# Kernel tuning notes

Hardware: AMD Instinct MI355X
Metric: run time of the kernel (lower is better)

Reference implementation:

```python
import jax, jax.numpy as jnp
import numpy as np

B, N, T, D, DG, DS, NC = 16, 64, 256, 64, 64, 9, 2

def _pe(times, d, max_len):
    # PositionalEncodingTF: timescales = max_len ** linspace(0,1,d//2)
    ts = jnp.asarray(max_len ** np.linspace(0.0, 1.0, d // 2), jnp.float32)
    st = times[..., None] / ts
    return jnp.concatenate([jnp.sin(st), jnp.cos(st)], -1)

def _ln(h, g, b):
    m = h.mean(-1, keepdims=True)
    v = ((h - m) ** 2).mean(-1, keepdims=True)
    return (h - m) * jax.lax.rsqrt(v + 1e-5) * g + b

def setup_inputs():
    key = jax.random.key(0)
    ks = jax.random.split(key, 40)
    s = 0.02
    value = jax.random.normal(ks[0], (B, T, N))
    obs = (jax.random.uniform(ks[1], (B, T, N)) < 0.5).astype(jnp.float32)
    times = jnp.sort(jax.random.uniform(ks[2], (B, T)) * T, axis=1)
    F = D + 2 * DG  # per-node GRU input feature size [x_t, h, time_enc]
    return dict(
        x=jnp.concatenate([value, obs, times[..., None]], -1),
        nufft=jax.random.normal(ks[3], (B, 2, T, N)),
        delta_t=jax.random.uniform(ks[4], (B, T)) * 0.1,
        static=jax.random.normal(ks[5], (B, DS)),
        lengths=jax.random.randint(ks[6], (B,), 1, T + 1),
        proj_w=jax.random.normal(ks[7], (2, D)) * s, proj_b=jnp.zeros(D),
        Wqkv=jax.random.normal(ks[8], (D, 3 * D)) * s, bqkv=jnp.zeros(3 * D),
        Wo=jax.random.normal(ks[9], (D, D)) * s, bo=jnp.zeros(D),
        ln1_g=jnp.ones(D), ln1_b=jnp.zeros(D),
        W1=jax.random.normal(ks[10], (D, D)) * s, b1=jnp.zeros(D),
        W2=jax.random.normal(ks[11], (D, D)) * s, b2=jnp.zeros(D),
        ln2_g=jnp.ones(D), ln2_b=jnp.zeros(D),
        WQ_f=jax.random.normal(ks[12], (T, T)) * 0.05,
        WK_f=jax.random.normal(ks[13], (T, T)) * 0.05,
        Wz=jax.random.normal(ks[14], (2 * F, DG)) * s, bz=jnp.zeros(DG),
        Wr=jax.random.normal(ks[15], (2 * F, DG)) * s, br=jnp.zeros(DG),
        Wc=jax.random.normal(ks[16], (2 * F, DG)) * s, bc=jnp.zeros(DG),
        Wfin=jax.random.normal(ks[17], (DG,)) * s, bfin=jnp.zeros(()),
        We=jax.random.normal(ks[18], (DS, N)) * s, be=jnp.zeros(N),
        Wc1=jax.random.normal(ks[19], (2 * N, 200)) * s, bc1=jnp.zeros(200),
        Wc2=jax.random.normal(ks[20], (200, NC)) * s, bc2=jnp.zeros(NC),
    )

def _forward(x, nufft, delta_t, static, lengths, proj_w, proj_b, Wqkv, bqkv, Wo, bo,
             ln1_g, ln1_b, W1, b1, W2, b2, ln2_g, ln2_b, WQ_f, WK_f,
             Wz, bz, Wr, br, Wc, bc, Wfin, bfin, We, be, Wc1, bc1, Wc2, bc2):
    lengths = jnp.maximum(lengths, 1)
    value = x[:, :, :N].transpose(0, 2, 1)          # (B,N,T)
    obs = x[:, :, N:2 * N].transpose(0, 2, 1)       # (B,N,T) observation mask
    times = x[:, :, -1]                              # (B,T)
    # Conv2d(2->D, 1x1) input projection == per-element linear over [value, mask]
    feat = jnp.stack([value, obs], -1) @ proj_w + proj_b   # (B,N,T,D)
    pe1 = _pe(times, D, T)                           # (B,T,D)
    tin = feat + pe1[:, None]                        # (B,N,T,D)
    # single-head transformer encoder layer (post-norm, relu FFN, eval: no dropout)
    qkv = tin @ Wqkv + bqkv
    q, k, v = jnp.split(qkv, 3, -1)
    scores = jnp.einsum('bnqd,bnkd->bnqk', q, k) / jnp.sqrt(jnp.float32(D))
    kpad = jnp.arange(T)[None, :] >= lengths[:, None]      # (B,T) key padding
    scores = jnp.where(kpad[:, None, None, :], -1e9, scores)
    attn = jax.nn.softmax(scores, -1)
    ao = jnp.einsum('bnqk,bnkd->bnqd', attn, v) @ Wo + bo
    h1 = _ln(tin + ao, ln1_g, ln1_b)
    ff = jax.nn.relu(h1 @ W1 + b1) @ W2 + b2
    tout = _ln(h1 + ff, ln2_g, ln2_b)
    m = obs[..., None]
    x_tat = m * tin + (1.0 - m) * tout               # masked blend (B,N,T,D)
    # Variable_Attention_layer on nufft channel 1: relu-score softmax attention
    xf = nufft[:, 1].transpose(0, 2, 1)              # (B,N,T)
    S = jax.nn.relu(jnp.einsum('bnt,bmt->bnm', xf @ WQ_f, xf @ WK_f)) / jnp.sqrt(jnp.float32(T))
    A = jax.nn.softmax(S, -1).mean(0)                # (N,N)
    A = 0.5 * (A + A.T)
    sm = jax.nn.softmax(A, -1)
    A = 0.5 * (sm + sm.T)
    pe2 = _pe(times, DG, T)                          # (B,T,DG)
    # graph-conv GRU over time (CGRNN) with delta_t decay + length masking
    def stepf(h, inputs):
        xt, tet, dtt, t = inputs                     # (B,N,D),(B,DG),(B,),()
        h = h * jnp.exp(-jax.nn.relu(dtt))[:, None, None]
        te = jnp.broadcast_to(tet[:, None, :], (h.shape[0], N, DG))
        inp = jnp.concatenate([xt, h, te], -1)
        gin = jnp.concatenate([inp, jnp.einsum('nm,bmf->bnf', A, inp)], -1)
        z = jax.nn.sigmoid(gin @ Wz + bz)
        r = jax.nn.sigmoid(gin @ Wr + br)
        inc = jnp.concatenate([xt, r * h, te], -1)
        cin = jnp.concatenate([inc, jnp.einsum('nm,bmf->bnf', A, inc)], -1)
        c = jnp.tanh(cin @ Wc + bc)
        hn = z * h + (1.0 - z) * c
        h = jnp.where((t < lengths)[:, None, None], hn, h)
        return h, None
    h0 = jnp.zeros((x.shape[0], N, DG), x.dtype)
    xs = (x_tat.transpose(2, 0, 1, 3), pe2.transpose(1, 0, 2), delta_t.T, jnp.arange(T))
    hT, _ = jax.lax.scan(stepf, h0, xs)
    out = hT @ Wfin + bfin                           # final 1x1 conv -> (B,N)
    emb = static @ We + be                           # (B,N)
    hcl = jax.nn.relu(jnp.concatenate([out, emb], -1) @ Wc1 + bc1)
    return hcl @ Wc2 + bc2                           # (B,NC)

def reference(x, nufft, delta_t, static, lengths, proj_w, proj_b, Wqkv, bqkv, Wo, bo,
              ln1_g, ln1_b, W1, b1, W2, b2, ln2_g, ln2_b, WQ_f, WK_f,
              Wz, bz, Wr, br, Wc, bc, Wfin, bfin, We, be, Wc1, bc1, Wc2, bc2):
    return _forward(x, nufft, delta_t, static, lengths, proj_w, proj_b, Wqkv, bqkv, Wo, bo,
                    ln1_g, ln1_b, W1, b1, W2, b2, ln2_g, ln2_b, WQ_f, WK_f,
                    Wz, bz, Wr, br, Wc, bc, Wfin, bfin, We, be, Wc1, bc1, Wc2, bc2)
```

## Files before the change

kernel.cpp:

```cpp
#include <hip/hip_runtime.h>
#include <hip/hip_bf16.h>
#include <cmath>

#define DEV __device__ __forceinline__

typedef short s16x8 __attribute__((ext_vector_type(8)));
typedef float f32x4 __attribute__((ext_vector_type(4)));

DEV unsigned short f2bu(float x){
  __hip_bfloat16 h = __float2bfloat16(x);
  return *reinterpret_cast<unsigned short*>(&h);
}
DEV float bs2f(unsigned short v){ return __uint_as_float(((unsigned)v)<<16); }
DEV float bs2f(short v){ return bs2f((unsigned short)v); }

DEV int swzo(int row, int col){
  return (row*128 + ((col*2) ^ ((row&7)<<4))) >> 1;
}
DEV s16x8 ldfrag(const short* tile, int t16, int lane, int kk){
  int row = t16 + (lane & 15);
  int c0  = (kk<<5) + ((lane>>4)<<3);
  int off = (row*128 + ((c0<<1) ^ ((row&7)<<4))) >> 1;
  return *(const s16x8*)(tile + off);
}
DEV int swzv(int d, int t){
  return (d*512 + ((t*2) ^ ((d&7)<<4))) >> 1;
}

__global__ void k0_prep(const float* __restrict__ Wqkv, const float* __restrict__ Wo,
                        const float* __restrict__ W1, const float* __restrict__ W2,
                        short* __restrict__ Wqkv_t, short* __restrict__ Wo_t,
                        short* __restrict__ W1_t, short* __restrict__ W2_t)
{
  int t = blockIdx.x*256 + threadIdx.x;
  if (t < 12288){ int nn=t>>6, k=t&63; Wqkv_t[t]=(short)f2bu(Wqkv[k*192+nn]); }
  else if (t < 16384){ int e=t-12288; int nn=e>>6,k=e&63; Wo_t[e]=(short)f2bu(Wo[k*64+nn]); }
  else if (t < 20480){ int e=t-16384; int nn=e>>6,k=e&63; W1_t[e]=(short)f2bu(W1[k*64+nn]); }
  else if (t < 24576){ int e=t-20480; int nn=e>>6,k=e&63; W2_t[e]=(short)f2bu(W2[k*64+nn]); }
}

__global__ void k1_pe_u(const float* __restrict__ x, const float* __restrict__ delta_t,
                        const float* __restrict__ Wz, const float* __restrict__ bz,
                        const float* __restrict__ Wr, const float* __restrict__ br,
                        const float* __restrict__ Wc, const float* __restrict__ bc,
                        float* __restrict__ pe, float* __restrict__ U, float* __restrict__ decay)
{
  const int bt = blockIdx.x;
  const int d  = threadIdx.x;
  __shared__ float pes[64];
  float tmv = x[(size_t)bt*129 + 128];
  int j = d & 31;
  float ts = (float)pow(256.0, (double)j * (1.0/31.0));
  float st = tmv / ts;
  float v = (d < 32) ? sinf(st) : cosf(st);
  pes[d] = v;
  pe[(size_t)bt*64 + d] = v;
  __syncthreads();
  float a0=bz[d], a1=0.f, a2=br[d], a3=0.f, a4=bc[d], a5=0.f;
  for (int k=0;k<64;k++){
    float p = pes[k];
    a0 = fmaf(p, Wz[(128+k)*64+d], a0);
    a1 = fmaf(p, Wz[(320+k)*64+d], a1);
    a2 = fmaf(p, Wr[(128+k)*64+d], a2);
    a3 = fmaf(p, Wr[(320+k)*64+d], a3);
    a4 = fmaf(p, Wc[(128+k)*64+d], a4);
    a5 = fmaf(p, Wc[(320+k)*64+d], a5);
  }
  float* u = U + (size_t)bt*384;
  u[d]=a0; u[64+d]=a1; u[128+d]=a2; u[192+d]=a3; u[256+d]=a4; u[320+d]=a5;
  if (d==0) decay[bt] = expf(-fmaxf(delta_t[bt], 0.f));
}

__global__ void k2a_qfkf(const float* __restrict__ nufft, const float* __restrict__ WQf,
                         const float* __restrict__ WKf, float* __restrict__ qf, float* __restrict__ kf)
{
  const int bn = blockIdx.x, b = bn>>6, n = bn&63;
  const int u = threadIdx.x;
  __shared__ float xs[256];
  xs[u] = nufft[ ((((size_t)b*2)+1)*256 + u)*64 + n ];
  __syncthreads();
  float aq=0.f, ak=0.f;
  for (int t=0;t<256;t++){
    float xv = xs[t];
    aq = fmaf(xv, WQf[t*256+u], aq);
    ak = fmaf(xv, WKf[t*256+u], ak);
  }
  qf[(size_t)bn*256+u]=aq;
  kf[(size_t)bn*256+u]=ak;
}

__launch_bounds__(256, 1)
__global__ void k2b_soft(const float* __restrict__ qf, const float* __restrict__ kf,
                         float* __restrict__ soft)
{
  const int b = blockIdx.x, tid = threadIdx.x;
  __shared__ float qs[64*257];
  __shared__ float ksh[64*257];
  __shared__ float Ss[64*65];
  const float* qb = qf + ((size_t)b<<14);
  const float* kb = kf + ((size_t)b<<14);
  for (int e=tid; e<16384; e+=256){
    int r=e>>8, c=e&255;
    qs[r*257+c]=qb[e];
    ksh[r*257+c]=kb[e];
  }
  __syncthreads();
  const int n = tid>>2, m0 = (tid&3)<<4;
  float acc[16];
  #pragma unroll
  for (int i=0;i<16;i++) acc[i]=0.f;
  for (int t=0;t<256;t++){
    float qv = qs[n*257+t];
    #pragma unroll
    for (int i=0;i<16;i++) acc[i] = fmaf(qv, ksh[(m0+i)*257+t], acc[i]);
  }
  #pragma unroll
  for (int i=0;i<16;i++) Ss[n*65+m0+i] = fmaxf(acc[i],0.f)*(1.f/16.f);
  __syncthreads();
  if (tid < 64){
    float mx=-1e30f;
    for (int m=0;m<64;m++) mx=fmaxf(mx, Ss[tid*65+m]);
    float s=0.f;
    for (int m=0;m<64;m++) s += expf(Ss[tid*65+m]-mx);
    float inv=1.f/s;
    for (int m=0;m<64;m++) soft[((size_t)b<<12)+(tid<<6)+m] = expf(Ss[tid*65+m]-mx)*inv;
  }
}

__global__ void k2c_A(const float* __restrict__ soft, short* __restrict__ Abf,
                      float* __restrict__ rs_out)
{
  const int tid = threadIdx.x;
  __shared__ float A0[64*65];
  __shared__ float A1[64*65];
  for (int e=tid; e<4096; e+=256){
    int nn=e>>6, mm=e&63;
    float s=0.f;
    #pragma unroll
    for (int b=0;b<16;b++) s += soft[((size_t)b<<12)+e];
    A0[nn*65+mm] = s*(1.f/16.f);
  }
  __syncthreads();
  for (int e=tid; e<4096; e+=256){
    int nn=e>>6, mm=e&63;
    A1[nn*65+mm] = 0.5f*(A0[nn*65+mm]+A0[mm*65+nn]);
  }
  __syncthreads();
  if (tid < 64){
    float mx=-1e30f;
    for (int m=0;m<64;m++) mx=fmaxf(mx, A1[tid*65+m]);
    float s=0.f;
    for (int m=0;m<64;m++) s += expf(A1[tid*65+m]-mx);
    float inv=1.f/s;
    for (int m=0;m<64;m++) A0[tid*65+m] = expf(A1[tid*65+m]-mx)*inv;
  }
  __syncthreads();
  for (int e=tid; e<4096; e+=256){
    int nn=e>>6, mm=e&63;
    float a = 0.5f*(A0[nn*65+mm]+A0[mm*65+nn]);
    A1[nn*65+mm] = a;
    Abf[e] = (short)f2bu(a);
  }
  __syncthreads();
  if (tid < 64){
    float s=0.f;
    for (int m=0;m<64;m++) s += A1[tid*65+m];
    rs_out[tid]=s;
  }
}

__launch_bounds__(512, 1)
__global__ void k3_former(const float* __restrict__ x, const float* __restrict__ pe_g,
    const float* __restrict__ proj_w, const float* __restrict__ proj_b,
    const short* __restrict__ Wqkv_t, const float* __restrict__ bqkv,
    const short* __restrict__ Wo_t, const float* __restrict__ bo,
    const float* __restrict__ ln1g, const float* __restrict__ ln1b,
    const short* __restrict__ W1_t, const float* __restrict__ b1,
    const short* __restrict__ W2_t, const float* __restrict__ b2,
    const float* __restrict__ ln2g, const float* __restrict__ ln2b,
    const int* __restrict__ lengths, unsigned short* __restrict__ xtat)
{
  const int bn = blockIdx.x, b = bn>>6, n = bn&63;
  const int tid = threadIdx.x, w = tid>>6, lane = tid&63;
  const int l15 = lane&15, lhi = lane>>4;
  __shared__ short tp_s[16384];
  __shared__ short q_s[16384];
  __shared__ short k_s[16384];
  __shared__ short v_t[16384];
  __shared__ float valr[256], obsr[256];

  int len = lengths[b]; if (len<1) len=1;
  const int LT = (len+15)>>4;
  const int KB = (len+63)>>6;

  if (tid < 256){
    const float* xr = x + ((size_t)b*256+tid)*129;
    valr[tid]=xr[n]; obsr[tid]=xr[64+n];
  }
  for (int e=tid; e<16384; e+=512) v_t[e]=0;
  __syncthreads();

  const int nrows = LT<<4;
  for (int e=tid; e<(nrows<<6); e+=512){
    int t=e>>6, d=e&63;
    float ti = fmaf(valr[t],proj_w[d], fmaf(obsr[t],proj_w[64+d], proj_b[d]))
             + pe_g[(((size_t)b<<8)+t)*64+d];
    tp_s[swzo(t,d)] = (short)f2bu(ti);
  }
  __syncthreads();

  #pragma unroll
  for (int j=0;j<2;j++){
    const int rt = w + (j<<3);
    if (rt < LT){
      s16x8 a0 = ldfrag(tp_s, rt<<4, lane, 0);
      s16x8 a1 = ldfrag(tp_s, rt<<4, lane, 1);
      const int rb = (rt<<4) + (lhi<<2);
      #pragma unroll
      for (int nt=0; nt<12; nt++){
        const short* wb = Wqkv_t + (((nt<<4)+l15)<<6) + (lhi<<3);
        s16x8 b0 = *(const s16x8*)wb;
        s16x8 b1v = *(const s16x8*)(wb+32);
        float bias = bqkv[(nt<<4)+l15];
        f32x4 acc = {bias,bias,bias,bias};
        acc = __builtin_amdgcn_mfma_f32_16x16x32_bf16(a0,b0,acc,0,0,0);
        acc = __builtin_amdgcn_mfma_f32_16x16x32_bf16(a1,b1v,acc,0,0,0);
        const int col = ((nt&3)<<4) + l15;
        if (nt<4){
          #pragma unroll
          for(int i=0;i<4;i++) q_s[swzo(rb+i,col)] = (short)f2bu(acc[i]*0.125f);
        } else if (nt<8){
          #pragma unroll
          for(int i=0;i<4;i++) k_s[swzo(rb+i,col)] = (short)f2bu(acc[i]);
        } else {
          #pragma unroll
          for(int i=0;i<4;i++) v_t[swzv(col, rb+i)] = (short)f2bu(acc[i]);
        }
      }
    }
  }
  __syncthreads();

  f32x4 Oac[2][4];
  float rsum[2][4];
  #pragma unroll
  for(int j=0;j<2;j++)
    #pragma unroll
    for(int dt=0;dt<4;dt++) Oac[j][dt]=(f32x4){0.f,0.f,0.f,0.f};
  #pragma unroll
  for(int j=0;j<2;j++)
    #pragma unroll
    for(int i=0;i<4;i++) rsum[j][i]=0.f;

  for (int kb=0; kb<KB; kb++){
    s16x8 kf[4][2];
    #pragma unroll
    for (int ct=0;ct<4;ct++){
      kf[ct][0]=ldfrag(k_s, (((kb<<2)+ct)<<4), lane, 0);
      kf[ct][1]=ldfrag(k_s, (((kb<<2)+ct)<<4), lane, 1);
    }
    #pragma unroll
    for (int j=0;j<2;j++){
      const int rt=w+(j<<3);
      if (rt < LT){
        s16x8 q0=ldfrag(q_s, rt<<4, lane, 0);
        s16x8 q1=ldfrag(q_s, rt<<4, lane, 1);
        const int rb=(rt<<4)+(lhi<<2);
        #pragma unroll
        for (int ct=0;ct<4;ct++){
          f32x4 s={0.f,0.f,0.f,0.f};
          s=__builtin_amdgcn_mfma_f32_16x16x32_bf16(q0,kf[ct][0],s,0,0,0);
          s=__builtin_amdgcn_mfma_f32_16x16x32_bf16(q1,kf[ct][1],s,0,0,0);
          const int key=(kb<<6)+(ct<<4)+l15;
          #pragma unroll
          for(int i=0;i<4;i++){
            float p = (key<len) ? __expf(s[i]) : 0.f;
            rsum[j][i]+=p;
            tp_s[swzo(rb+i,(ct<<4)+l15)] = (short)f2bu(p);
          }
        }
      }
    }
    __syncthreads();
    s16x8 vf[4][2];
    #pragma unroll
    for (int dt=0;dt<4;dt++){
      const int d=(dt<<4)+l15;
      #pragma unroll
      for (int kk=0;kk<2;kk++){
        const int k0=(kk<<5)+(lhi<<3);
        vf[dt][kk] = *(const s16x8*)(v_t + swzv(d, (kb<<6)+k0));
      }
    }
    #pragma unroll
    for (int j=0;j<2;j++){
      const int rt=w+(j<<3);
      if (rt < LT){
        s16x8 p0=ldfrag(tp_s, rt<<4, lane, 0);
        s16x8 p1=ldfrag(tp_s, rt<<4, lane, 1);
        #pragma unroll
        for (int dt=0;dt<4;dt++){
          Oac[j][dt]=__builtin_amdgcn_mfma_f32_16x16x32_bf16(p0,vf[dt][0],Oac[j][dt],0,0,0);
          Oac[j][dt]=__builtin_amdgcn_mfma_f32_16x16x32_bf16(p1,vf[dt][1],Oac[j][dt],0,0,0);
        }
      }
    }
    __syncthreads();
  }

  float inv[2][4];
  #pragma unroll
  for(int j=0;j<2;j++)
    #pragma unroll
    for(int i=0;i<4;i++){
      float v=rsum[j][i];
      v += __shfl_xor(v,1); v += __shfl_xor(v,2); v += __shfl_xor(v,4); v += __shfl_xor(v,8);
      inv[j][i]=1.f/v;
    }

  #pragma unroll
  for (int j=0;j<2;j++){
    const int rt=w+(j<<3);
    if (rt < LT){
      const int rb=(rt<<4)+(lhi<<2);
      #pragma unroll
      for (int dt=0;dt<4;dt++)
        #pragma unroll
        for (int i=0;i<4;i++)
          q_s[swzo(rb+i,(dt<<4)+l15)] = (short)f2bu(Oac[j][dt][i]*inv[j][i]);
    }
  }
  __syncthreads();

  f32x4 h1[2][4];
  #pragma unroll
  for (int j=0;j<2;j++){
    const int rt=w+(j<<3);
    if (rt < LT){
      s16x8 a0=ldfrag(q_s, rt<<4, lane, 0);
      s16x8 a1=ldfrag(q_s, rt<<4, lane, 1);
      const int rb=(rt<<4)+(lhi<<2);
      #pragma unroll
      for (int dt=0;dt<4;dt++){
        const int col=(dt<<4)+l15;
        const short* wb = Wo_t + (col<<6) + (lhi<<3);
        s16x8 b0=*(const s16x8*)wb, b1v=*(const s16x8*)(wb+32);
        float bias=bo[col];
        f32x4 acc={bias,bias,bias,bias};
        acc=__builtin_amdgcn_mfma_f32_16x16x32_bf16(a0,b0,acc,0,0,0);
        acc=__builtin_amdgcn_mfma_f32_16x16x32_bf16(a1,b1v,acc,0,0,0);
        #pragma unroll
        for(int i=0;i<4;i++){
          const int row=rb+i;
          acc[i]+= fmaf(valr[row],proj_w[col], fmaf(obsr[row],proj_w[64+col], proj_b[col]))
                 + pe_g[(((size_t)b<<8)+row)*64+col];
        }
        h1[j][dt]=acc;
      }
      f32x4 mu, rsq;
      #pragma unroll
      for(int i=0;i<4;i++){
        float sv = h1[j][0][i]+h1[j][1][i]+h1[j][2][i]+h1[j][3][i];
        sv += __shfl_xor(sv,1); sv+=__shfl_xor(sv,2); sv+=__shfl_xor(sv,4); sv+=__shfl_xor(sv,8);
        mu[i]=sv*(1.f/64.f);
      }
      #pragma unroll
      for(int i=0;i<4;i++){
        float sv=0.f;
        #pragma unroll
        for(int dt=0;dt<4;dt++){ float c=h1[j][dt][i]-mu[i]; sv=fmaf(c,c,sv); }
        sv += __shfl_xor(sv,1); sv+=__shfl_xor(sv,2); sv+=__shfl_xor(sv,4); sv+=__shfl_xor(sv,8);
        rsq[i]=1.f/sqrtf(sv*(1.f/64.f)+1e-5f);
      }
      #pragma unroll
      for(int dt=0;dt<4;dt++){
        const int col=(dt<<4)+l15;
        float g=ln1g[col], bb=ln1b[col];
        #pragma unroll
        for(int i=0;i<4;i++){
          float hv=(h1[j][dt][i]-mu[i])*rsq[i]*g+bb;
          h1[j][dt][i]=hv;
          k_s[swzo(rb+i,col)] = (short)f2bu(hv);
        }
      }
    }
  }
  __syncthreads();

  #pragma unroll
  for (int j=0;j<2;j++){
    const int rt=w+(j<<3);
    if (rt < LT){
      s16x8 a0=ldfrag(k_s, rt<<4, lane, 0);
      s16x8 a1=ldfrag(k_s, rt<<4, lane, 1);
      const int rb=(rt<<4)+(lhi<<2);
      #pragma unroll
      for (int dt=0;dt<4;dt++){
        const int col=(dt<<4)+l15;
        const short* wb = W1_t + (col<<6)+(lhi<<3);
        s16x8 b0=*(const s16x8*)wb, b1v=*(const s16x8*)(wb+32);
        float bias=b1[col];
        f32x4 acc={bias,bias,bias,bias};
        acc=__builtin_amdgcn_mfma_f32_16x16x32_bf16(a0,b0,acc,0,0,0);
        acc=__builtin_amdgcn_mfma_f32_16x16x32_bf16(a1,b1v,acc,0,0,0);
        #pragma unroll
        for(int i=0;i<4;i++) tp_s[swzo(rb+i,col)]=(short)f2bu(fmaxf(acc[i],0.f));
      }
    }
  }
  __syncthreads();

  #pragma unroll
  for (int j=0;j<2;j++){
    const int rt=w+(j<<3);
    if (rt < LT){
      s16x8 a0=ldfrag(tp_s, rt<<4, lane, 0);
      s16x8 a1=ldfrag(tp_s, rt<<4, lane, 1);
      const int rb=(rt<<4)+(lhi<<2);
      f32x4 to[4];
      #pragma unroll
      for (int dt=0;dt<4;dt++){
        const int col=(dt<<4)+l15;
        const short* wb = W2_t + (col<<6)+(lhi<<3);
        s16x8 b0=*(const s16x8*)wb, b1v=*(const s16x8*)(wb+32);
        float bias=b2[col];
        f32x4 acc={bias,bias,bias,bias};
        acc=__builtin_amdgcn_mfma_f32_16x16x32_bf16(a0,b0,acc,0,0,0);
        acc=__builtin_amdgcn_mfma_f32_16x16x32_bf16(a1,b1v,acc,0,0,0);
        acc += h1[j][dt];
        to[dt]=acc;
      }
      f32x4 mu, rsq;
      #pragma unroll
      for(int i=0;i<4;i++){
        float sv = to[0][i]+to[1][i]+to[2][i]+to[3][i];
        sv += __shfl_xor(sv,1); sv+=__shfl_xor(sv,2); sv+=__shfl_xor(sv,4); sv+=__shfl_xor(sv,8);
        mu[i]=sv*(1.f/64.f);
      }
      #pragma unroll
      for(int i=0;i<4;i++){
        float sv=0.f;
        #pragma unroll
        for(int dt=0;dt<4;dt++){ float c=to[dt][i]-mu[i]; sv=fmaf(c,c,sv); }
        sv += __shfl_xor(sv,1); sv+=__shfl_xor(sv,2); sv+=__shfl_xor(sv,4); sv+=__shfl_xor(sv,8);
        rsq[i]=1.f/sqrtf(sv*(1.f/64.f)+1e-5f);
      }
      #pragma unroll
      for(int dt=0;dt<4;dt++){
        const int col=(dt<<4)+l15;
        float g=ln2g[col], bb=ln2b[col];
        #pragma unroll
        for(int i=0;i<4;i++){
          const int row=rb+i;
          if (row < len){
            float tv=(to[dt][i]-mu[i])*rsq[i]*g+bb;
            float tin = fmaf(valr[row],proj_w[col], fmaf(obsr[row],proj_w[64+col], proj_b[col]))
                      + pe_g[(((size_t)b<<8)+row)*64+col];
            float ob = obsr[row];
            xtat[((size_t)bn<<14)+(row<<6)+col] = f2bu(ob*tin + (1.f-ob)*tv);
          }
        }
      }
    }
  }
}

__launch_bounds__(512, 1)
__global__ void k4_scan(const unsigned short* __restrict__ xtat, const float* __restrict__ U,
                        const float* __restrict__ decay, const short* __restrict__ Abf,
                        const float* __restrict__ rs_g,
                        const float* __restrict__ Wz, const float* __restrict__ Wr,
                        const float* __restrict__ Wc,
                        const int* __restrict__ lengths, float* __restrict__ hT)
{
  const int b = blockIdx.x;
  const int tid = threadIdx.x;
  const int w = tid >> 6, lane = tid & 63;
  const int tn = w & 3, tm0 = (w >> 2) << 1;
  const int colg = (tn<<4) + (lane & 15);
  const int rsub = (lane >> 4) << 2;

  __shared__ short h_rm[4096], h_tp[4096], xt_rm[4096], xt_tp[4096];
  __shared__ short rh_rm[4096], rh_tp[4096], axt_s[4096], ah_s[4096], arh_s[4096];
  __shared__ float dec_s[256];
  __shared__ float rs_s[64];

  int len = lengths[b]; if (len < 1) len = 1;
  for (int e=tid; e<256; e+=512) dec_s[e] = decay[b*256+e];
  if (tid < 64) rs_s[tid] = rs_g[tid];

  s16x8 aA[2][2];
  #pragma unroll
  for (int ti=0;ti<2;ti++)
    #pragma unroll
    for (int kk=0;kk<2;kk++)
      aA[ti][kk] = *(const s16x8*)(Abf + (((tm0+ti)<<4) + (lane&15))*64 + (kk<<5) + ((lane>>4)<<3));

  s16x8 wf[12][2];
  {
    const float* Wg[3] = {Wz, Wr, Wc};
    const int offs[4] = {0, 64, 192, 256};
    #pragma unroll
    for (int g3=0; g3<3; g3++)
      #pragma unroll
      for (int s4=0; s4<4; s4++)
        #pragma unroll
        for (int kk=0; kk<2; kk++){
          s16x8 tf;
          int kb = (kk<<5) + ((lane>>4)<<3);
          #pragma unroll
          for (int j=0;j<8;j++)
            tf[j] = (short)f2bu(Wg[g3][(offs[s4]+kb+j)*64 + colg]);
          wf[g3*4+s4][kk] = tf;
        }
  }

  f32x4 hreg[2] = {{0.f,0.f,0.f,0.f},{0.f,0.f,0.f,0.f}};
  const int xn  = tid >> 3;
  const int xd0 = (tid & 7) << 3;
  __syncthreads();

  for (int t=0; t<256; t++){
    float dc = dec_s[t];
    #pragma unroll
    for (int ti=0;ti<2;ti++)
      #pragma unroll
      for (int i=0;i<4;i++) hreg[ti][i] *= dc;

    if (t < len){
      #pragma unroll
      for (int ti=0;ti<2;ti++){
        int rb = ((tm0+ti)<<4) + rsub;
        #pragma unroll
        for (int i=0;i<4;i++){
          short hv = (short)f2bu(hreg[ti][i]);
          h_rm[swzo(rb+i, colg)] = hv;
          h_tp[swzo(colg, rb+i)] = hv;
        }
      }
      {
        const s16x8 vv = *(const s16x8*)((const short*)xtat + (((size_t)(b*64+xn))*256 + t)*64 + xd0);
        *(s16x8*)(xt_rm + swzo(xn, xd0)) = vv;
        #pragma unroll
        for (int j=0;j<8;j++) xt_tp[swzo(xd0+j, xn)] = vv[j];
      }
      __syncthreads();

      {
        f32x4 ax[2] = {{0,0,0,0},{0,0,0,0}}, ahh[2] = {{0,0,0,0},{0,0,0,0}};
        #pragma unroll
        for (int kk=0;kk<2;kk++){
          s16x8 bx = ldfrag(xt_tp, tn<<4, lane, kk);
          s16x8 bh = ldfrag(h_tp,  tn<<4, lane, kk);
          #pragma unroll
          for (int ti=0;ti<2;ti++){
            ax[ti]  = __builtin_amdgcn_mfma_f32_16x16x32_bf16(aA[ti][kk], bx, ax[ti], 0,0,0);
            ahh[ti] = __builtin_amdgcn_mfma_f32_16x16x32_bf16(aA[ti][kk], bh, ahh[ti], 0,0,0);
          }
        }
        #pragma unroll
        for (int ti=0;ti<2;ti++){
          int rb = ((tm0+ti)<<4) + rsub;
          #pragma unroll
          for (int i=0;i<4;i++){
            axt_s[swzo(rb+i, colg)] = (short)f2bu(ax[ti][i]);
            ah_s [swzo(rb+i, colg)] = (short)f2bu(ahh[ti][i]);
          }
        }
      }
      __syncthreads();

      const float* ub = U + ((size_t)(b*256+t))*384;
      float u1z=ub[colg], u2z=ub[64+colg], u1r=ub[128+colg], u2r=ub[192+colg];
      float u1c=ub[256+colg], u2c=ub[320+colg];

      f32x4 gz[2] = {{0,0,0,0},{0,0,0,0}}, gr[2] = {{0,0,0,0},{0,0,0,0}};
      #pragma unroll
      for (int ti=0;ti<2;ti++){
        int rt = (tm0+ti)<<4;
        #pragma unroll
        for (int kk=0;kk<2;kk++){
          s16x8 fxt = ldfrag(xt_rm, rt, lane, kk);
          s16x8 fh  = ldfrag(h_rm,  rt, lane, kk);
          s16x8 fax = ldfrag(axt_s, rt, lane, kk);
          s16x8 fah = ldfrag(ah_s,  rt, lane, kk);
          gz[ti] = __builtin_amdgcn_mfma_f32_16x16x32_bf16(fxt, wf[0][kk], gz[ti], 0,0,0);
          gz[ti] = __builtin_amdgcn_mfma_f32_16x16x32_bf16(fh,  wf[1][kk], gz[ti], 0,0,0);
          gz[ti] = __builtin_amdgcn_mfma_f32_16x16x32_bf16(fax, wf[2][kk], gz[ti], 0,0,0);
          gz[ti] = __builtin_amdgcn_mfma_f32_16x16x32_bf16(fah, wf[3][kk], gz[ti], 0,0,0);
          gr[ti] = __builtin_amdgcn_mfma_f32_16x16x32_bf16(fxt, wf[4][kk], gr[ti], 0,0,0);
          gr[ti] = __builtin_amdgcn_mfma_f32_16x16x32_bf16(fh,  wf[5][kk], gr[ti], 0,0,0);
          gr[ti] = __builtin_amdgcn_mfma_f32_16x16x32_bf16(fax, wf[6][kk], gr[ti], 0,0,0);
          gr[ti] = __builtin_amdgcn_mfma_f32_16x16x32_bf16(fah, wf[7][kk], gr[ti], 0,0,0);
        }
      }
      f32x4 zz[2];
      #pragma unroll
      for (int ti=0;ti<2;ti++){
        int rb = ((tm0+ti)<<4) + rsub;
        #pragma unroll
        for (int i=0;i<4;i++){
          float rsv = rs_s[rb+i];
          float gzv = gz[ti][i] + u1z + rsv*u2z;
          float grv = gr[ti][i] + u1r + rsv*u2r;
          float zv = 1.f/(1.f+__expf(-gzv));
          float rv = 1.f/(1.f+__expf(-grv));
          zz[ti][i] = zv;
          short rhv = (short)f2bu(rv * hreg[ti][i]);
          rh_rm[swzo(rb+i, colg)] = rhv;
          rh_tp[swzo(colg, rb+i)] = rhv;
        }
      }
      __syncthreads();

      {
        f32x4 ar[2] = {{0,0,0,0},{0,0,0,0}};
        #pragma unroll
        for (int kk=0;kk<2;kk++){
          s16x8 brh = ldfrag(rh_tp, tn<<4, lane, kk);
          #pragma unroll
          for (int ti=0;ti<2;ti++)
            ar[ti] = __builtin_amdgcn_mfma_f32_16x16x32_bf16(aA[ti][kk], brh, ar[ti], 0,0,0);
        }
        #pragma unroll
        for (int ti=0;ti<2;ti++){
          int rb = ((tm0+ti)<<4) + rsub;
          #pragma unroll
          for (int i=0;i<4;i++)
            arh_s[swzo(rb+i, colg)] = (short)f2bu(ar[ti][i]);
        }
      }
      __syncthreads();

      {
        f32x4 gc[2] = {{0,0,0,0},{0,0,0,0}};
        #pragma unroll
        for (int ti=0;ti<2;ti++){
          int rt = (tm0+ti)<<4;
          #pragma unroll
          for (int kk=0;kk<2;kk++){
            s16x8 fxt = ldfrag(xt_rm, rt, lane, kk);
            s16x8 frh = ldfrag(rh_rm, rt, lane, kk);
            s16x8 fax = ldfrag(axt_s, rt, lane, kk);
            s16x8 far = ldfrag(arh_s, rt, lane, kk);
            gc[ti] = __builtin_amdgcn_mfma_f32_16x16x32_bf16(fxt, wf[8][kk],  gc[ti], 0,0,0);
            gc[ti] = __builtin_amdgcn_mfma_f32_16x16x32_bf16(frh, wf[9][kk],  gc[ti], 0,0,0);
            gc[ti] = __builtin_amdgcn_mfma_f32_16x16x32_bf16(fax, wf[10][kk], gc[ti], 0,0,0);
            gc[ti] = __builtin_amdgcn_mfma_f32_16x16x32_bf16(far, wf[11][kk], gc[ti], 0,0,0);
          }
        }
        #pragma unroll
        for (int ti=0;ti<2;ti++){
          int rb = ((tm0+ti)<<4) + rsub;
          #pragma unroll
          for (int i=0;i<4;i++){
            float rsv = rs_s[rb+i];
            float gcv = gc[ti][i] + u1c + rsv*u2c;
            float cv = 1.f - 2.f/(__expf(2.f*gcv)+1.f);
            float zv = zz[ti][i];
            hreg[ti][i] = zv*hreg[ti][i] + (1.f-zv)*cv;
          }
        }
      }
      __syncthreads();
    }
  }

  #pragma unroll
  for (int ti=0;ti<2;ti++){
    int rb = ((tm0+ti)<<4) + rsub;
    #pragma unroll
    for (int i=0;i<4;i++)
      hT[(((size_t)b<<6) + rb + i)*64 + colg] = hreg[ti][i];
  }
}

__global__ void k5_head(const float* __restrict__ hT, const float* __restrict__ Wfin,
                        const float* __restrict__ bfin,
                        const float* __restrict__ stat, const float* __restrict__ We,
                        const float* __restrict__ be,
                        const float* __restrict__ Wc1, const float* __restrict__ bc1,
                        const float* __restrict__ Wc2, const float* __restrict__ bc2,
                        float* __restrict__ out)
{
  const int b = blockIdx.x, tid = threadIdx.x;
  __shared__ float cat[128];
  __shared__ float hcl[200];
  if (tid < 64){
    const float* hr = hT + (((size_t)b<<6)+tid)*64;
    float a = bfin[0];
    #pragma unroll
    for (int d=0;d<64;d++) a = fmaf(hr[d], Wfin[d], a);
    cat[tid]=a;
  } else if (tid < 128){
    int nn = tid-64;
    float a = be[nn];
    #pragma unroll
    for (int k=0;k<9;k++) a = fmaf(stat[b*9+k], We[k*64+nn], a);
    cat[tid]=a;
  }
  __syncthreads();
  if (tid < 200){
    float a = bc1[tid];
    for (int k=0;k<128;k++) a = fmaf(cat[k], Wc1[k*200+tid], a);
    hcl[tid] = fmaxf(a, 0.f);
  }
  __syncthreads();
  if (tid < 2){
    float a = bc2[tid];
    for (int k=0;k<200;k++) a = fmaf(hcl[k], Wc2[k*2+tid], a);
    out[b*2+tid] = a;
  }
}

extern "C" void kernel_launch(void* const* d_in, const int* in_sizes, int n_in,
                              void* d_out, int out_size, void* d_ws, size_t ws_size,
                              hipStream_t stream)
{
  const float* x       = (const float*)d_in[0];
  const float* nufft   = (const float*)d_in[1];
  const float* delta_t = (const float*)d_in[2];
  const float* stat    = (const float*)d_in[3];
  const int*   lengths = (const int*)  d_in[4];
  const float* proj_w  = (const float*)d_in[5];
  const float* proj_b  = (const float*)d_in[6];
  const float* Wqkv    = (const float*)d_in[7];
  const float* bqkv    = (const float*)d_in[8];
  const float* Wo      = (const float*)d_in[9];
  const float* bo      = (const float*)d_in[10];
  const float* ln1g    = (const float*)d_in[11];
  const float* ln1b    = (const float*)d_in[12];
  const float* W1      = (const float*)d_in[13];
  const float* b1      = (const float*)d_in[14];
  const float* W2      = (const float*)d_in[15];
  const float* b2      = (const float*)d_in[16];
  const float* ln2g    = (const float*)d_in[17];
  const float* ln2b    = (const float*)d_in[18];
  const float* WQf     = (const float*)d_in[19];
  const float* WKf     = (const float*)d_in[20];
  const float* Wz      = (const float*)d_in[21];
  const float* bz      = (const float*)d_in[22];
  const float* Wr      = (const float*)d_in[23];
  const float* br      = (const float*)d_in[24];
  const float* Wc      = (const float*)d_in[25];
  const float* bc      = (const float*)d_in[26];
  const float* Wfin    = (const float*)d_in[27];
  const float* bfin    = (const float*)d_in[28];
  const float* We      = (const float*)d_in[29];
  const float* be      = (const float*)d_in[30];
  const float* Wc1     = (const float*)d_in[31];
  const float* bc1     = (const float*)d_in[32];
  const float* Wc2     = (const float*)d_in[33];
  const float* bc2     = (const float*)d_in[34];
  float* out = (float*)d_out;

  char* ws = (char*)d_ws;
  size_t o = 0;
  float* pe    = (float*)(ws+o); o += (size_t)4096*64*4;
  float* U     = (float*)(ws+o); o += (size_t)4096*384*4;
  float* decay = (float*)(ws+o); o += (size_t)4096*4;
  unsigned short* xtat = (unsigned short*)(ws+o); o += (size_t)1024*256*64*2;
  float* qf    = (float*)(ws+o); o += (size_t)1024*256*4;
  float* kf    = (float*)(ws+o); o += (size_t)1024*256*4;
  float* soft  = (float*)(ws+o); o += (size_t)16*4096*4;
  short* Abf   = (short*)(ws+o); o += (size_t)4096*2;
  float* rs    = (float*)(ws+o); o += (size_t)64*4;
  float* hT    = (float*)(ws+o); o += (size_t)16*64*64*4;
  short* Wqkv_t= (short*)(ws+o); o += (size_t)12288*2;
  short* Wo_t  = (short*)(ws+o); o += (size_t)4096*2;
  short* W1_t  = (short*)(ws+o); o += (size_t)4096*2;
  short* W2_t  = (short*)(ws+o); o += (size_t)4096*2;
  (void)ws_size; (void)in_sizes; (void)n_in; (void)out_size;

  hipLaunchKernelGGL(k0_prep,   dim3(96),   dim3(256), 0, stream,
                     Wqkv, Wo, W1, W2, Wqkv_t, Wo_t, W1_t, W2_t);
  hipLaunchKernelGGL(k1_pe_u,   dim3(4096), dim3(64),  0, stream,
                     x, delta_t, Wz, bz, Wr, br, Wc, bc, pe, U, decay);
  hipLaunchKernelGGL(k2a_qfkf,  dim3(1024), dim3(256), 0, stream,
                     nufft, WQf, WKf, qf, kf);
  hipLaunchKernelGGL(k2b_soft,  dim3(16),   dim3(256), 0, stream, qf, kf, soft);
  hipLaunchKernelGGL(k2c_A,     dim3(1),    dim3(256), 0, stream, soft, Abf, rs);
  hipLaunchKernelGGL(k3_former, dim3(1024), dim3(512), 0, stream,
                     x, pe, proj_w, proj_b, Wqkv_t, bqkv, Wo_t, bo, ln1g, ln1b,
                     W1_t, b1, W2_t, b2, ln2g, ln2b, lengths, xtat);
  hipLaunchKernelGGL(k4_scan,   dim3(16),   dim3(512), 0, stream,
                     xtat, U, decay, Abf, rs, Wz, Wr, Wc, lengths, hT);
  hipLaunchKernelGGL(k5_head,   dim3(16),   dim3(256), 0, stream,
                     hT, Wfin, bfin, stat, We, be, Wc1, bc1, Wc2, bc2, out);
}
```

Before: 1.069 ms.

## Hoist x-dependent GRU gate projections out of the sequential scan into a parallel kernel

A new kernel, k35_xg, computes the input-side gate contributions (x_t and A·x_t times the z, r and c weights) for all timesteps in parallel across 4096 blocks and writes them to a bf16 buffer. The sequential scan now only does the hidden-state MFMAs and prefetches the next step's precomputed gates and U terms into registers. It loops only to len and applies the remaining decay product at the end. It also drops one LDS round trip and uses vector stores for the transposes. This shortens the serial critical path of a kernel that runs only 16 blocks, at the cost of an extra ~100MB workspace buffer, a launch, and extra bf16 rounding of the precomputed gates.

```diff
diff --git a/kernel.cpp b/kernel.cpp
--- a/kernel.cpp
+++ b/kernel.cpp
@@ -5,6 +5,7 @@
 #define DEV __device__ __forceinline__
 
 typedef short s16x8 __attribute__((ext_vector_type(8)));
+typedef short s16x4 __attribute__((ext_vector_type(4)));
 typedef float f32x4 __attribute__((ext_vector_type(4)));
 
 DEV unsigned short f2bu(float x){
@@ -29,14 +30,23 @@
 
 __global__ void k0_prep(const float* __restrict__ Wqkv, const float* __restrict__ Wo,
                         const float* __restrict__ W1, const float* __restrict__ W2,
+                        const float* __restrict__ Wz, const float* __restrict__ Wr,
+                        const float* __restrict__ Wc,
                         short* __restrict__ Wqkv_t, short* __restrict__ Wo_t,
-                        short* __restrict__ W1_t, short* __restrict__ W2_t)
+                        short* __restrict__ W1_t, short* __restrict__ W2_t,
+                        short* __restrict__ Wg_t)
 {
   int t = blockIdx.x*256 + threadIdx.x;
   if (t < 12288){ int nn=t>>6, k=t&63; Wqkv_t[t]=(short)f2bu(Wqkv[k*192+nn]); }
   else if (t < 16384){ int e=t-12288; int nn=e>>6,k=e&63; Wo_t[e]=(short)f2bu(Wo[k*64+nn]); }
   else if (t < 20480){ int e=t-16384; int nn=e>>6,k=e&63; W1_t[e]=(short)f2bu(W1[k*64+nn]); }
   else if (t < 24576){ int e=t-20480; int nn=e>>6,k=e&63; W2_t[e]=(short)f2bu(W2[k*64+nn]); }
+  else if (t < 49152){
+    int e=t-24576;
+    int g=e>>13, rem=e&8191, s=rem>>12, rem2=rem&4095, c=rem2>>6, k=rem2&63;
+    const float* Wg = (g==0)?Wz:((g==1)?Wr:Wc);
+    Wg_t[e] = (short)f2bu(Wg[((s?192:0)+k)*64 + c]);
+  }
 }
 
 __global__ void k1_pe_u(const float* __restrict__ x, const float* __restrict__ delta_t,
@@ -50,7 +60,7 @@
   __shared__ float pes[64];
   float tmv = x[(size_t)bt*129 + 128];
   int j = d & 31;
-  float ts = (float)pow(256.0, (double)j * (1.0/31.0));
+  float ts = exp2f((float)j * (8.0f/31.0f));
   float st = tmv / ts;
   float v = (d < 32) ? sinf(st) : cosf(st);
   pes[d] = v;
@@ -465,8 +475,82 @@
   }
 }
 
+__global__ void k35_xg(const unsigned short* __restrict__ xtat, const short* __restrict__ Abf,
+                       const short* __restrict__ Wg_t, const int* __restrict__ lengths,
+                       unsigned short* __restrict__ Xall)
+{
+  const int bt = blockIdx.x, b = bt>>8, t = bt&255;
+  int len = lengths[b]; if (len<1) len=1;
+  if (t >= len) return;
+  const int tid = threadIdx.x, w = tid>>6, lane = tid&63;
+  const int l15 = lane&15, lhi = lane>>4;
+  __shared__ short xt_rm[4096], xt_tp[4096], axt_rm[4096];
+
+  #pragma unroll
+  for (int q=0;q<2;q++){
+    int e = tid + (q<<8);
+    int nn = e>>3, c0 = (e&7)<<3;
+    s16x8 v = *(const s16x8*)((const short*)xtat + (((size_t)(b*64+nn)*256 + t)<<6) + c0);
+    *(s16x8*)(xt_rm + swzo(nn,c0)) = v;
+    #pragma unroll
+    for (int jj=0;jj<8;jj++) xt_tp[swzo(c0+jj, nn)] = v[jj];
+  }
+  __syncthreads();
+
+  {
+    s16x8 bx[2];
+    #pragma unroll
+    for (int kk=0;kk<2;kk++) bx[kk]=ldfrag(xt_tp, w<<4, lane, kk);
+    #pragma unroll
+    for (int rt=0;rt<4;rt++){
+      f32x4 acc={0.f,0.f,0.f,0.f};
+      #pragma unroll
+      for (int kk=0;kk<2;kk++){
+        s16x8 af = *(const s16x8*)(Abf + ((rt<<4)+l15)*64 + (kk<<5) + (lhi<<3));
+        acc=__builtin_amdgcn_mfma_f32_16x16x32_bf16(af,bx[kk],acc,0,0,0);
+      }
+      const int rb=(rt<<4)+(lhi<<2);
+      #pragma unroll
+      for(int i=0;i<4;i++) axt_rm[swzo(rb+i,(w<<4)+l15)] = (short)f2bu(acc[i]);
+    }
+  }
+  __syncthreads();
+
+  s16x8 fx[4][2], fa[4][2];
+  #pragma unroll
+  for (int rt=0;rt<4;rt++)
+    #pragma unroll
+    for (int kk=0;kk<2;kk++){
+      fx[rt][kk]=ldfrag(xt_rm, rt<<4, lane, kk);
+      fa[rt][kk]=ldfrag(axt_rm, rt<<4, lane, kk);
+    }
+  const int col = (w<<4)+l15;
+  #pragma unroll
+  for (int g=0; g<3; g++){
+    s16x8 wbx[2], wba[2];
+    #pragma unroll
+    for (int kk=0;kk<2;kk++){
+      wbx[kk] = *(const s16x8*)(Wg_t + (((g<<1)  )*64 + col)*64 + (kk<<5)+(lhi<<3));
+      wba[kk] = *(const s16x8*)(Wg_t + (((g<<1)+1)*64 + col)*64 + (kk<<5)+(lhi<<3));
+    }
+    #pragma unroll
+    for (int rt=0;rt<4;rt++){
+      f32x4 acc={0.f,0.f,0.f,0.f};
+      #pragma unroll
+      for (int kk=0;kk<2;kk++){
+        acc=__builtin_amdgcn_mfma_f32_16x16x32_bf16(fx[rt][kk],wbx[kk],acc,0,0,0);
+        acc=__builtin_amdgcn_mfma_f32_16x16x32_bf16(fa[rt][kk],wba[kk],acc,0,0,0);
+      }
+      s16x4 pk;
+      #pragma unroll
+      for(int i=0;i<4;i++) pk[i]=(short)f2bu(acc[i]);
+      *(s16x4*)((short*)Xall + ((size_t)(bt*3+g)<<12) + (col<<6) + (rt<<4)+(lhi<<2)) = pk;
+    }
+  }
+}
+
 __launch_bounds__(512, 1)
-__global__ void k4_scan(const unsigned short* __restrict__ xtat, const float* __restrict__ U,
+__global__ void k4_scan(const unsigned short* __restrict__ Xall, const float* __restrict__ U,
                         const float* __restrict__ decay, const short* __restrict__ Abf,
                         const float* __restrict__ rs_g,
                         const float* __restrict__ Wz, const float* __restrict__ Wr,
@@ -477,198 +561,206 @@
   const int tid = threadIdx.x;
   const int w = tid >> 6, lane = tid & 63;
   const int tn = w & 3, tm0 = (w >> 2) << 1;
-  const int colg = (tn<<4) + (lane & 15);
-  const int rsub = (lane >> 4) << 2;
-
-  __shared__ short h_rm[4096], h_tp[4096], xt_rm[4096], xt_tp[4096];
-  __shared__ short rh_rm[4096], rh_tp[4096], axt_s[4096], ah_s[4096], arh_s[4096];
+  const int l15 = lane & 15, lhi = lane >> 4;
+  const int colg = (tn<<4) + l15;
+  const int rsub = lhi << 2;
+
+  __shared__ short h_rm[4096], h_tp[4096], rh_rm[4096], rh_tp[4096];
+  __shared__ short ah_rm[4096], arh_rm[4096];
   __shared__ float dec_s[256];
-  __shared__ float rs_s[64];
 
   int len = lengths[b]; if (len < 1) len = 1;
   for (int e=tid; e<256; e+=512) dec_s[e] = decay[b*256+e];
-  if (tid < 64) rs_s[tid] = rs_g[tid];
+
+  int rb0 = (tm0<<4) + rsub, rb1 = ((tm0+1)<<4) + rsub;
+  f32x4 rs4[2];
+  rs4[0] = *(const f32x4*)(rs_g + rb0);
+  rs4[1] = *(const f32x4*)(rs_g + rb1);
 
   s16x8 aA[2][2];
   #pragma unroll
   for (int ti=0;ti<2;ti++)
     #pragma unroll
     for (int kk=0;kk<2;kk++)
-      aA[ti][kk] = *(const s16x8*)(Abf + (((tm0+ti)<<4) + (lane&15))*64 + (kk<<5) + ((lane>>4)<<3));
-
-  s16x8 wf[12][2];
+      aA[ti][kk] = *(const s16x8*)(Abf + (((tm0+ti)<<4) + l15)*64 + (kk<<5) + (lhi<<3));
+
+  s16x8 wf[3][2][2];
   {
     const float* Wg[3] = {Wz, Wr, Wc};
-    const int offs[4] = {0, 64, 192, 256};
-    #pragma unroll
-    for (int g3=0; g3<3; g3++)
-      #pragma unroll
-      for (int s4=0; s4<4; s4++)
+    #pragma unroll
+    for (int g=0; g<3; g++)
+      #pragma unroll
+      for (int s=0; s<2; s++)
         #pragma unroll
         for (int kk=0; kk<2; kk++){
           s16x8 tf;
-          int kb = (kk<<5) + ((lane>>4)<<3);
+          int kb = (kk<<5) + (lhi<<3);
           #pragma unroll
           for (int j=0;j<8;j++)
-            tf[j] = (short)f2bu(Wg[g3][(offs[s4]+kb+j)*64 + colg]);
-          wf[g3*4+s4][kk] = tf;
+            tf[j] = (short)f2bu(Wg[g][((s?256:64)+kb+j)*64 + colg]);
+          wf[g][s][kk] = tf;
         }
   }
 
   f32x4 hreg[2] = {{0.f,0.f,0.f,0.f},{0.f,0.f,0.f,0.f}};
-  const int xn  = tid >> 3;
-  const int xd0 = (tid & 7) << 3;
-  __syncthreads();
-
-  for (int t=0; t<256; t++){
+
+  const short* Xb = (const short*)Xall + ((size_t)(b*256)*3<<12);
+  s16x4 xc[6]; float uc[6];
+  {
+    const short* xp = Xb;
+    #pragma unroll
+    for (int g=0;g<3;g++){
+      xc[g*2+0] = *(const s16x4*)(xp + ((size_t)g<<12) + (colg<<6) + rb0);
+      xc[g*2+1] = *(const s16x4*)(xp + ((size_t)g<<12) + (colg<<6) + rb1);
+    }
+    const float* ub = U + (size_t)(b*256)*384;
+    #pragma unroll
+    for (int q=0;q<6;q++) uc[q] = ub[q*64 + colg];
+  }
+  __syncthreads();
+
+  for (int t=0; t<len; t++){
     float dc = dec_s[t];
     #pragma unroll
     for (int ti=0;ti<2;ti++)
       #pragma unroll
       for (int i=0;i<4;i++) hreg[ti][i] *= dc;
 
-    if (t < len){
+    #pragma unroll
+    for (int ti=0;ti<2;ti++){
+      int rb = ti ? rb1 : rb0;
+      s16x4 hp;
+      #pragma unroll
+      for (int i=0;i<4;i++){
+        short hv = (short)f2bu(hreg[ti][i]);
+        h_rm[swzo(rb+i, colg)] = hv;
+        hp[i] = hv;
+      }
+      *(s16x4*)(h_tp + swzo(colg, rb)) = hp;
+    }
+
+    s16x4 xn[6]; float un[6];
+    #pragma unroll
+    for (int q=0;q<6;q++){ xn[q]=(s16x4){0,0,0,0}; un[q]=0.f; }
+    if (t+1 < len){
+      const short* xp = Xb + ((size_t)(t+1)*3<<12);
+      #pragma unroll
+      for (int g=0;g<3;g++){
+        xn[g*2+0] = *(const s16x4*)(xp + ((size_t)g<<12) + (colg<<6) + rb0);
+        xn[g*2+1] = *(const s16x4*)(xp + ((size_t)g<<12) + (colg<<6) + rb1);
+      }
+      const float* ub = U + (size_t)(b*256+t+1)*384;
+      #pragma unroll
+      for (int q=0;q<6;q++) un[q] = ub[q*64 + colg];
+    }
+    __syncthreads();
+
+    {
+      f32x4 ah[2] = {{0,0,0,0},{0,0,0,0}};
+      #pragma unroll
+      for (int kk=0;kk<2;kk++){
+        s16x8 bh = ldfrag(h_tp, tn<<4, lane, kk);
+        #pragma unroll
+        for (int ti=0;ti<2;ti++)
+          ah[ti] = __builtin_amdgcn_mfma_f32_16x16x32_bf16(aA[ti][kk], bh, ah[ti], 0,0,0);
+      }
       #pragma unroll
       for (int ti=0;ti<2;ti++){
-        int rb = ((tm0+ti)<<4) + rsub;
-        #pragma unroll
-        for (int i=0;i<4;i++){
-          short hv = (short)f2bu(hreg[ti][i]);
-          h_rm[swzo(rb+i, colg)] = hv;
-          h_tp[swzo(colg, rb+i)] = hv;
-        }
-      }
-      {
-        const s16x8 vv = *(const s16x8*)((const short*)xtat + (((size_t)(b*64+xn))*256 + t)*64 + xd0);
-        *(s16x8*)(xt_rm + swzo(xn, xd0)) = vv;
-        #pragma unroll
-        for (int j=0;j<8;j++) xt_tp[swzo(xd0+j, xn)] = vv[j];
-      }
-      __syncthreads();
-
-      {
-        f32x4 ax[2] = {{0,0,0,0},{0,0,0,0}}, ahh[2] = {{0,0,0,0},{0,0,0,0}};
-        #pragma unroll
-        for (int kk=0;kk<2;kk++){
-          s16x8 bx = ldfrag(xt_tp, tn<<4, lane, kk);
-          s16x8 bh = ldfrag(h_tp,  tn<<4, lane, kk);
-          #pragma unroll
-          for (int ti=0;ti<2;ti++){
-            ax[ti]  = __builtin_amdgcn_mfma_f32_16x16x32_bf16(aA[ti][kk], bx, ax[ti], 0,0,0);
-            ahh[ti] = __builtin_amdgcn_mfma_f32_16x16x32_bf16(aA[ti][kk], bh, ahh[ti], 0,0,0);
-          }
-        }
-        #pragma unroll
-        for (int ti=0;ti<2;ti++){
-          int rb = ((tm0+ti)<<4) + rsub;
-          #pragma unroll
-          for (int i=0;i<4;i++){
-            axt_s[swzo(rb+i, colg)] = (short)f2bu(ax[ti][i]);
-            ah_s [swzo(rb+i, colg)] = (short)f2bu(ahh[ti][i]);
-          }
-        }
-      }
-      __syncthreads();
-
-      const float* ub = U + ((size_t)(b*256+t))*384;
-      float u1z=ub[colg], u2z=ub[64+colg], u1r=ub[128+colg], u2r=ub[192+colg];
-      float u1c=ub[256+colg], u2c=ub[320+colg];
-
-      f32x4 gz[2] = {{0,0,0,0},{0,0,0,0}}, gr[2] = {{0,0,0,0},{0,0,0,0}};
+        int rb = ti ? rb1 : rb0;
+        #pragma unroll
+        for (int i=0;i<4;i++) ah_rm[swzo(rb+i, colg)] = (short)f2bu(ah[ti][i]);
+      }
+    }
+    __syncthreads();
+
+    f32x4 zz[2];
+    #pragma unroll
+    for (int ti=0;ti<2;ti++){
+      int rt = (tm0+ti)<<4;
+      int rb = ti ? rb1 : rb0;
+      f32x4 gz, gr;
+      #pragma unroll
+      for (int i=0;i<4;i++){
+        gz[i] = bs2f(xc[ti][i])   + uc[0] + rs4[ti][i]*uc[1];
+        gr[i] = bs2f(xc[2+ti][i]) + uc[2] + rs4[ti][i]*uc[3];
+      }
+      #pragma unroll
+      for (int kk=0;kk<2;kk++){
+        s16x8 fh = ldfrag(h_rm,  rt, lane, kk);
+        s16x8 fa = ldfrag(ah_rm, rt, lane, kk);
+        gz = __builtin_amdgcn_mfma_f32_16x16x32_bf16(fh, wf[0][0][kk], gz, 0,0,0);
+        gz = __builtin_amdgcn_mfma_f32_16x16x32_bf16(fa, wf[0][1][kk], gz, 0,0,0);
+        gr = __builtin_amdgcn_mfma_f32_16x16x32_bf16(fh, wf[1][0][kk], gr, 0,0,0);
+        gr = __builtin_amdgcn_mfma_f32_16x16x32_bf16(fa, wf[1][1][kk], gr, 0,0,0);
+      }
+      s16x4 rhp;
+      #pragma unroll
+      for (int i=0;i<4;i++){
+        float zv = 1.f/(1.f+__expf(-gz[i]));
+        float rv = 1.f/(1.f+__expf(-gr[i]));
+        zz[ti][i] = zv;
+        short rhv = (short)f2bu(rv * hreg[ti][i]);
+        rh_rm[swzo(rb+i, colg)] = rhv;
+        rhp[i] = rhv;
+      }
+      *(s16x4*)(rh_tp + swzo(colg, rb)) = rhp;
+    }
+    __syncthreads();
+
+    {
+      f32x4 ar[2] = {{0,0,0,0},{0,0,0,0}};
+      #pragma unroll
+      for (int kk=0;kk<2;kk++){
+        s16x8 brh = ldfrag(rh_tp, tn<<4, lane, kk);
+        #pragma unroll
+        for (int ti=0;ti<2;ti++)
+          ar[ti] = __builtin_amdgcn_mfma_f32_16x16x32_bf16(aA[ti][kk], brh, ar[ti], 0,0,0);
+      }
       #pragma unroll
       for (int ti=0;ti<2;ti++){
-        int rt = (tm0+ti)<<4;
-        #pragma unroll
-        for (int kk=0;kk<2;kk++){
-          s16x8 fxt = ldfrag(xt_rm, rt, lane, kk);
-          s16x8 fh  = ldfrag(h_rm,  rt, lane, kk);
-          s16x8 fax = ldfrag(axt_s, rt, lane, kk);
-          s16x8 fah = ldfrag(ah_s,  rt, lane, kk);
-          gz[ti] = __builtin_amdgcn_mfma_f32_16x16x32_bf16(fxt, wf[0][kk], gz[ti], 0,0,0);
-          gz[ti] = __builtin_amdgcn_mfma_f32_16x16x32_bf16(fh,  wf[1][kk], gz[ti], 0,0,0);
-          gz[ti] = __builtin_amdgcn_mfma_f32_16x16x32_bf16(fax, wf[2][kk], gz[ti], 0,0,0);
-          gz[ti] = __builtin_amdgcn_mfma_f32_16x16x32_bf16(fah, wf[3][kk], gz[ti], 0,0,0);
-          gr[ti] = __builtin_amdgcn_mfma_f32_16x16x32_bf16(fxt, wf[4][kk], gr[ti], 0,0,0);
-          gr[ti] = __builtin_amdgcn_mfma_f32_16x16x32_bf16(fh,  wf[5][kk], gr[ti], 0,0,0);
-          gr[ti] = __builtin_amdgcn_mfma_f32_16x16x32_bf16(fax, wf[6][kk], gr[ti], 0,0,0);
-          gr[ti] = __builtin_amdgcn_mfma_f32_16x16x32_bf16(fah, wf[7][kk], gr[ti], 0,0,0);
-        }
-      }
-      f32x4 zz[2];
-      #pragma unroll
-      for (int ti=0;ti<2;ti++){
-        int rb = ((tm0+ti)<<4) + rsub;
-        #pragma unroll
-        for (int i=0;i<4;i++){
-          float rsv = rs_s[rb+i];
-          float gzv = gz[ti][i] + u1z + rsv*u2z;
-          float grv = gr[ti][i] + u1r + rsv*u2r;
-          float zv = 1.f/(1.f+__expf(-gzv));
-          float rv = 1.f/(1.f+__expf(-grv));
-          zz[ti][i] = zv;
-          short rhv = (short)f2bu(rv * hreg[ti][i]);
-          rh_rm[swzo(rb+i, colg)] = rhv;
-          rh_tp[swzo(colg, rb+i)] = rhv;
-        }
-      }
-      __syncthreads();
-
-      {
-        f32x4 ar[2] = {{0,0,0,0},{0,0,0,0}};
-        #pragma unroll
-        for (int kk=0;kk<2;kk++){
-          s16x8 brh = ldfrag(rh_tp, tn<<4, lane, kk);
-          #pragma unroll
-          for (int ti=0;ti<2;ti++)
-            ar[ti] = __builtin_amdgcn_mfma_f32_16x16x32_bf16(aA[ti][kk], brh, ar[ti], 0,0,0);
-        }
-        #pragma unroll
-        for (int ti=0;ti<2;ti++){
-          int rb = ((tm0+ti)<<4) + rsub;
-          #pragma unroll
-          for (int i=0;i<4;i++)
-            arh_s[swzo(rb+i, colg)] = (short)f2bu(ar[ti][i]);
-        }
-      }
-      __syncthreads();
-
-      {
-        f32x4 gc[2] = {{0,0,0,0},{0,0,0,0}};
-        #pragma unroll
-        for (int ti=0;ti<2;ti++){
-          int rt = (tm0+ti)<<4;
-          #pragma unroll
-          for (int kk=0;kk<2;kk++){
-            s16x8 fxt = ldfrag(xt_rm, rt, lane, kk);
-            s16x8 frh = ldfrag(rh_rm, rt, lane, kk);
-            s16x8 fax = ldfrag(axt_s, rt, lane, kk);
-            s16x8 far = ldfrag(arh_s, rt, lane, kk);
-            gc[ti] = __builtin_amdgcn_mfma_f32_16x16x32_bf16(fxt, wf[8][kk],  gc[ti], 0,0,0);
-            gc[ti] = __builtin_amdgcn_mfma_f32_16x16x32_bf16(frh, wf[9][kk],  gc[ti], 0,0,0);
-            gc[ti] = __builtin_amdgcn_mfma_f32_16x16x32_bf16(fax, wf[10][kk], gc[ti], 0,0,0);
-            gc[ti] = __builtin_amdgcn_mfma_f32_16x16x32_bf16(far, wf[11][kk], gc[ti], 0,0,0);
-          }
-        }
-        #pragma unroll
-        for (int ti=0;ti<2;ti++){
-          int rb = ((tm0+ti)<<4) + rsub;
-          #pragma unroll
-          for (int i=0;i<4;i++){
-            float rsv = rs_s[rb+i];
-            float gcv = gc[ti][i] + u1c + rsv*u2c;
-            float cv = 1.f - 2.f/(__expf(2.f*gcv)+1.f);
-            float zv = zz[ti][i];
-            hreg[ti][i] = zv*hreg[ti][i] + (1.f-zv)*cv;
-          }
-        }
-      }
-      __syncthreads();
-    }
-  }
+        int rb = ti ? rb1 : rb0;
+        #pragma unroll
+        for (int i=0;i<4;i++) arh_rm[swzo(rb+i, colg)] = (short)f2bu(ar[ti][i]);
+      }
+    }
+    __syncthreads();
+
+    #pragma unroll
+    for (int ti=0;ti<2;ti++){
+      int rt = (tm0+ti)<<4;
+      f32x4 gc;
+      #pragma unroll
+      for (int i=0;i<4;i++)
+        gc[i] = bs2f(xc[4+ti][i]) + uc[4] + rs4[ti][i]*uc[5];
+      #pragma unroll
+      for (int kk=0;kk<2;kk++){
+        s16x8 frh = ldfrag(rh_rm,  rt, lane, kk);
+        s16x8 far = ldfrag(arh_rm, rt, lane, kk);
+        gc = __builtin_amdgcn_mfma_f32_16x16x32_bf16(frh, wf[2][0][kk], gc, 0,0,0);
+        gc = __builtin_amdgcn_mfma_f32_16x16x32_bf16(far, wf[2][1][kk], gc, 0,0,0);
+      }
+      #pragma unroll
+      for (int i=0;i<4;i++){
+        float cv = 1.f - 2.f/(__expf(2.f*gc[i])+1.f);
+        float zv = zz[ti][i];
+        hreg[ti][i] = zv*hreg[ti][i] + (1.f-zv)*cv;
+      }
+    }
+
+    #pragma unroll
+    for (int q=0;q<6;q++){ xc[q]=xn[q]; uc[q]=un[q]; }
+  }
+
+  float sp = 1.f;
+  for (int t=len; t<256; t++) sp *= dec_s[t];
+  #pragma unroll
+  for (int ti=0;ti<2;ti++)
+    #pragma unroll
+    for (int i=0;i<4;i++) hreg[ti][i] *= sp;
 
   #pragma unroll
   for (int ti=0;ti<2;ti++){
-    int rb = ((tm0+ti)<<4) + rsub;
+    int rb = ti ? rb1 : rb0;
     #pragma unroll
     for (int i=0;i<4;i++)
       hT[(((size_t)b<<6) + rb + i)*64 + colg] = hreg[ti][i];
@@ -770,10 +862,12 @@
   short* Wo_t  = (short*)(ws+o); o += (size_t)4096*2;
   short* W1_t  = (short*)(ws+o); o += (size_t)4096*2;
   short* W2_t  = (short*)(ws+o); o += (size_t)4096*2;
+  short* Wg_t  = (short*)(ws+o); o += (size_t)24576*2;
+  unsigned short* Xall = (unsigned short*)(ws+o); o += (size_t)4096*3*4096*2;
   (void)ws_size; (void)in_sizes; (void)n_in; (void)out_size;
 
-  hipLaunchKernelGGL(k0_prep,   dim3(96),   dim3(256), 0, stream,
-                     Wqkv, Wo, W1, W2, Wqkv_t, Wo_t, W1_t, W2_t);
+  hipLaunchKernelGGL(k0_prep,   dim3(192),  dim3(256), 0, stream,
+                     Wqkv, Wo, W1, W2, Wz, Wr, Wc, Wqkv_t, Wo_t, W1_t, W2_t, Wg_t);
   hipLaunchKernelGGL(k1_pe_u,   dim3(4096), dim3(64),  0, stream,
                      x, delta_t, Wz, bz, Wr, br, Wc, bc, pe, U, decay);
   hipLaunchKernelGGL(k2a_qfkf,  dim3(1024), dim3(256), 0, stream,
@@ -783,8 +877,10 @@
   hipLaunchKernelGGL(k3_former, dim3(1024), dim3(512), 0, stream,
                      x, pe, proj_w, proj_b, Wqkv_t, bqkv, Wo_t, bo, ln1g, ln1b,
                      W1_t, b1, W2_t, b2, ln2g, ln2b, lengths, xtat);
+  hipLaunchKernelGGL(k35_xg,    dim3(4096), dim3(256), 0, stream,
+                     xtat, Abf, Wg_t, lengths, Xall);
   hipLaunchKernelGGL(k4_scan,   dim3(16),   dim3(512), 0, stream,
-                     xtat, U, decay, Abf, rs, Wz, Wr, Wc, lengths, hT);
+                     Xall, U, decay, Abf, rs, Wz, Wr, Wc, lengths, hT);
   hipLaunchKernelGGL(k5_head,   dim3(16),   dim3(256), 0, stream,
                      hT, Wfin, bfin, stat, We, be, Wc1, bc1, Wc2, bc2, out);
 }
```

Result: no change. 1.072 ms (+0.3%).
